# Optimization experiments

Hardware: AMD Instinct MI355X
Metric: run time of the kernel (lower is better)

## Reference

```python
import jax, jax.numpy as jnp
import numpy as np
from jax import lax

DN3D = ('NDHWC', 'DHWIO', 'NDHWC')


def _conv3d(x, w):
    return lax.conv_general_dilated(x, w, window_strides=(1, 1, 1),
                                    padding='VALID', dimension_numbers=DN3D)


def _cconv3d(xr, xi, wr, wi):
    # (xr + i xi) * (wr + i wi)
    yr = _conv3d(xr, wr) - _conv3d(xi, wi)
    yi = _conv3d(xr, wi) + _conv3d(xi, wr)
    return yr, yi


def _project(wr, wi, zero_mean):
    # zero-mean + bound-norm weight projection over (kD,kH,kW,Cin) per output filter
    ax = (0, 1, 2, 3)
    if zero_mean:
        wr = wr - jnp.mean(wr, ax, keepdims=True)
        wi = wi - jnp.mean(wi, ax, keepdims=True)
    norm = jnp.sqrt(jnp.sum(wr * wr + wi * wi, ax, keepdims=True))
    s = 1.0 / jnp.maximum(norm, 1.0)
    return wr * s, wi * s


def _sympad(x, pads):
    # pads: list of (lo, hi) per axis
    return jnp.pad(x, pads, mode='symmetric')


def setup_inputs() -> dict:
    key = jax.random.key(0)
    ks = jax.random.split(key, 6)
    B, T, Z, Y, X, C = 2, 8, 20, 64, 64, 2
    F1, F = 32, 32
    return {
        'xr': jax.random.normal(ks[0], (B, T, Z, Y, X, C), jnp.float32),
        'xi': jax.random.normal(ks[1], (B, T, Z, Y, X, C), jnp.float32),
        'wxyz_r': jax.random.normal(ks[2], (3, 3, 3, C, F1), jnp.float32) * 0.1,
        'wxyz_i': jax.random.normal(ks[3], (3, 3, 3, C, F1), jnp.float32) * 0.1,
        'wt_r': jax.random.normal(ks[4], (3, 1, 1, F1, F), jnp.float32) * 0.1,
        'wt_i': jax.random.normal(ks[5], (3, 1, 1, F1, F), jnp.float32) * 0.1,
    }


def reference(xr, xi, wxyz_r, wxyz_i, wt_r, wt_i):
    B, T, Z, Y, X, C = xr.shape
    kz, ky, kx = wxyz_r.shape[0], wxyz_r.shape[1], wxyz_r.shape[2]
    kt = wt_r.shape[0]
    F1 = wxyz_r.shape[-1]
    F = wt_r.shape[-1]

    # projected (zero-mean, bound-norm) complex kernels
    wsr, wsi = _project(wxyz_r, wxyz_i, zero_mean=True)
    wtr, wti = _project(wt_r, wt_i, zero_mean=False)

    # --- spatial 3D conv over (Z,Y,X): fold T into batch (== per-T-slice loop)
    sr = xr.reshape(B * T, Z, Y, X, C)
    si = xi.reshape(B * T, Z, Y, X, C)
    pads_sp = [(0, 0), (kz // 2, kz // 2), (ky // 2, ky // 2), (kx // 2, kx // 2), (0, 0)]
    sr = _sympad(sr, pads_sp)
    si = _sympad(si, pads_sp)
    spr, spi = _cconv3d(sr, si, wsr, wsi)          # [B*T, Z, Y, X, F1]
    spr = spr.reshape(B, T, Z, Y, X, F1)
    spi = spi.reshape(B, T, Z, Y, X, F1)

    # --- temporal conv (kt,1,1) over (T,Z,Y): fold X into batch (== per-X-slice loop)
    tr = spr.transpose(0, 4, 1, 2, 3, 5).reshape(B * X, T, Z, Y, F1)
    ti = spi.transpose(0, 4, 1, 2, 3, 5).reshape(B * X, T, Z, Y, F1)
    pads_t = [(0, 0), (kt // 2, kt // 2), (0, 0), (0, 0), (0, 0)]
    tr = _sympad(tr, pads_t)
    ti = _sympad(ti, pads_t)
    ytr, yti = _cconv3d(tr, ti, wtr, wti)          # [B*X, T, Z, Y, F]
    yr = ytr.reshape(B, X, T, Z, Y, F).transpose(0, 2, 3, 4, 1, 5)
    yi = yti.reshape(B, X, T, Z, Y, F).transpose(0, 2, 3, 4, 1, 5)
    return yr, yi
```

## Files before the change

### kernel.cpp

```cpp
#include <hip/hip_runtime.h>

#define B_ 2
#define T_ 8
#define Z_ 20
#define Y_ 64
#define X_ 64
#define C_ 2
#define F1_ 32
#define F_ 32

constexpr int NPTS = B_*T_*Z_*Y_*X_;
constexpr int ZYX  = Z_*Y_*X_;

constexpr int RING_STRIDE = 36;
constexpr int SLOT_DW     = 16*RING_STRIDE;
constexpr int HALO2       = 3*3*34;

using bf8   = __attribute__((ext_vector_type(8))) short;
using f32x4 = __attribute__((ext_vector_type(4))) float;

__device__ inline unsigned short f2bf(float x) {
    unsigned u = __builtin_bit_cast(unsigned, x);
    return (unsigned short)((u + 0x7fff + ((u >> 16) & 1)) >> 16);
}
__device__ inline unsigned pk(float a, float b) {
    return (unsigned)f2bf(a) | ((unsigned)f2bf(b) << 16);
}

__global__ __launch_bounds__(64) void project_kernel(
    const float* __restrict__ wxr, const float* __restrict__ wxi,
    const float* __restrict__ wtr, const float* __restrict__ wti,
    float* __restrict__ psr, float* __restrict__ psi,
    float* __restrict__ otr, float* __restrict__ oti)
{
    const int bid  = blockIdx.x;
    const int lane = threadIdx.x;

    if (bid < F1_) {
        const int f = bid;
        float er = 0.f, ei = 0.f;
        if (lane < 54) { er = wxr[lane*F1_ + f]; ei = wxi[lane*F1_ + f]; }
        float sr = er, si = ei;
        #pragma unroll
        for (int o = 32; o >= 1; o >>= 1) { sr += __shfl_xor(sr, o); si += __shfl_xor(si, o); }
        const float mr = sr * (1.f/54.f), mi = si * (1.f/54.f);
        const float dr = er - mr, di = ei - mi;
        float sq = (lane < 54) ? (dr*dr + di*di) : 0.f;
        #pragma unroll
        for (int o = 32; o >= 1; o >>= 1) sq += __shfl_xor(sq, o);
        const float s = 1.f / fmaxf(sqrtf(sq), 1.f);
        if (lane < 54) { psr[lane*F1_ + f] = dr*s; psi[lane*F1_ + f] = di*s; }
    } else {
        const int f = bid - F1_;
        float er[2], ei[2];
        float sq = 0.f;
        #pragma unroll
        for (int k = 0; k < 2; ++k) {
            const int e = lane + k*64;
            if (e < 96) { er[k] = wtr[e*F_ + f]; ei[k] = wti[e*F_ + f]; sq += er[k]*er[k] + ei[k]*ei[k]; }
            else        { er[k] = 0.f;  ei[k] = 0.f; }
        }
        #pragma unroll
        for (int o = 32; o >= 1; o >>= 1) sq += __shfl_xor(sq, o);
        const float s = 1.f / fmaxf(sqrtf(sq), 1.f);
        #pragma unroll
        for (int k = 0; k < 2; ++k) {
            const int e = lane + k*64;
            if (e < 96) { otr[e*F_ + f] = er[k]*s; oti[e*F_ + f] = ei[k]*s; }
        }
    }
}

__global__ __launch_bounds__(256) void pack_kernel(
    const float* __restrict__ psr, const float* __restrict__ psi,
    const float* __restrict__ ptr_, const float* __restrict__ pti,
    unsigned short* __restrict__ wsp, unsigned short* __restrict__ wp)
{
    const int g = blockIdx.x;
    if (g < 16) {
        for (int o = g*512 + threadIdx.x; o < (g+1)*512; o += 256) {
            const int j  = o & 7;
            const int l  = (o >> 3) & 63;
            const int gg = o >> 9;
            const int kb = gg & 3, ct = gg >> 2;
            const int k  = kb*32 + (l >> 4)*8 + j;
            const int n  = ct*16 + (l & 15);
            float v = 0.f;
            if (k < 108) {
                const int tap = k >> 2, q = k & 3, cin = q & 1, cp = q >> 1;
                const int f  = n & 31;
                const float wr = psr[(tap*2 + cin)*F1_ + f];
                const float wi = psi[(tap*2 + cin)*F1_ + f];
                v = (n < 32) ? (cp ? -wi : wr) : (cp ? wr : wi);
            }
            wsp[o] = f2bf(v);
        }
    } else {
        for (int o = (g-16)*512 + threadIdx.x; o < (g-15)*512; o += 256) {
            const int j  = o & 7;
            const int l  = (o >> 3) & 63;
            const int gg = o >> 9;
            const int kb = gg % 6, ct = gg / 6;
            const int k  = kb*32 + (l >> 4)*8 + j;
            const int n  = ct*16 + (l & 15);
            const int kt = k >> 6, f1 = (k >> 1) & 31, c = k & 1;
            const int f  = n & 31;
            const float wr = ptr_[(kt*F1_ + f1)*F_ + f];
            const float wi = pti[(kt*F1_ + f1)*F_ + f];
            const float v  = (n < 32) ? (c ? -wi : wr) : (c ? wr : wi);
            wp[o] = f2bf(v);
        }
    }
}

__global__ __launch_bounds__(256) void repack_kernel(
    const float* __restrict__ xr, const float* __restrict__ xi,
    uint2* __restrict__ xb)
{
    const int p = blockIdx.x*256 + threadIdx.x;
    const float2 vr = *reinterpret_cast<const float2*>(xr + (size_t)p*2);
    const float2 vi = *reinterpret_cast<const float2*>(xi + (size_t)p*2);
    uint2 v;
    v.x = (unsigned)f2bf(vr.x) | ((unsigned)f2bf(vr.y) << 16);
    v.y = (unsigned)f2bf(vi.x) | ((unsigned)f2bf(vi.y) << 16);
    xb[p] = v;
}

__global__ __launch_bounds__(256, 2) void fused_kernel(
    const uint2* __restrict__ xb,
    const unsigned short* __restrict__ wsp,
    const unsigned short* __restrict__ wp,
    float* __restrict__ yr, float* __restrict__ yi)
{
    __shared__ uint4 ring4[4*2*3*SLOT_DW/4];
    __shared__ uint2 slab[4][2][HALO2];
    unsigned* ring = reinterpret_cast<unsigned*>(ring4);

    const int tid  = threadIdx.x;
    const int lane = tid & 63;
    const int wid  = tid >> 6;
    const int lx   = lane & 15;
    const int lg   = lane >> 4;

    const int bq    = blockIdx.x;
    const int ypair = bq & 31;
    const int z     = (bq >> 5) % Z_;
    const int b     = bq / (32*Z_);
    const int y     = ypair*2 + (wid >> 1);
    const int x0    = (wid & 1) * 32;

    bf8 wsf[4][4];
    const bf8* w8 = reinterpret_cast<const bf8*>(wsp);
    #pragma unroll
    for (int ct = 0; ct < 4; ++ct)
        #pragma unroll
        for (int kb = 0; kb < 4; ++kb)
            wsf[ct][kb] = w8[(ct*4 + kb)*64 + lane];

    bf8 wtf[4][6];
    const bf8* wp8 = reinterpret_cast<const bf8*>(wp);
    #pragma unroll
    for (int ct = 0; ct < 4; ++ct)
        #pragma unroll
        for (int kb = 0; kb < 6; ++kb)
            wtf[ct][kb] = wp8[(ct*6 + kb)*64 + lane];

    int xoff[5];
    #pragma unroll
    for (int i = 0; i < 5; ++i) {
        int it = lane + i*64; if (it >= HALO2) it = HALO2-1;
        const int iz = it / 102;
        const int iy = (it / 34) % 3;
        const int ix = it % 34;
        int zz = z + iz - 1;  zz = zz < 0 ? 0 : (zz >= Z_ ? Z_-1 : zz);
        int yy = y + iy - 1;  yy = yy < 0 ? 0 : (yy >= Y_ ? Y_-1 : yy);
        int xx = x0 + ix - 1; xx = xx < 0 ? 0 : (xx >= X_ ? X_-1 : xx);
        xoff[i] = (zz*Y_ + yy)*X_ + xx;
    }

    int o8[4][2];
    #pragma unroll
    for (int kb = 0; kb < 4; ++kb)
        #pragma unroll
        for (int s = 0; s < 2; ++s) {
            int ta = kb*8 + lg*2 + s; if (ta > 26) ta = 26;
            const int dz = ta/9, dyx = ta - dz*9, dy = dyx/3, dx = dyx - dy*3;
            o8[kb][s] = (dz*3 + dy)*34 + dx + lx;
        }

    unsigned* myring  = ring + wid*(2*3*SLOT_DW);
    const int  rbase  = lx*RING_STRIDE + lg*4;
    const size_t orow = (((size_t)b*T_)*Z_ + z)*(size_t)(Y_*X_) + (size_t)y*X_ + x0 + lx;

    uint4 caLo, caHi, cbLo, cbHi;
    uint2 stmp[5];

    auto STAGE_ISSUE = [&](int t) {
        const uint2* xt = xb + (size_t)(b*T_ + t)*ZYX;
        #pragma unroll
        for (int i = 0; i < 4; ++i) stmp[i] = xt[xoff[i]];
        if (lane < HALO2 - 256) stmp[4] = xt[xoff[4]];
    };
    auto STAGE_WRITE = [&](int bufsel) {
        uint2* s = slab[wid][bufsel];
        #pragma unroll
        for (int i = 0; i < 4; ++i) s[lane + i*64] = stmp[i];
        if (lane < HALO2 - 256) s[lane + 256] = stmp[4];
    };

    auto SPATIAL = [&](int bufsel, int xadd, uint4& lo, uint4& hi) {
        const uint2* s = slab[wid][bufsel];
        bf8 af[4];
        #pragma unroll
        for (int kb = 0; kb < 4; ++kb) {
            const uint2 l2 = s[o8[kb][0] + xadd];
            const uint2 h2 = s[o8[kb][1] + xadd];
            af[kb] = __builtin_bit_cast(bf8, make_uint4(l2.x, l2.y, h2.x, h2.y));
        }
        f32x4 acc[4];
        #pragma unroll
        for (int ct = 0; ct < 4; ++ct) acc[ct] = (f32x4){0.f,0.f,0.f,0.f};
        #pragma unroll
        for (int ct = 0; ct < 4; ++ct)
            #pragma unroll
            for (int kb = 0; kb < 4; ++kb)
                acc[ct] = __builtin_amdgcn_mfma_f32_16x16x32_bf16(
                              wsf[ct][kb], af[kb], acc[ct], 0, 0, 0);
        lo = make_uint4(pk(acc[0][0],acc[2][0]), pk(acc[0][1],acc[2][1]),
                        pk(acc[0][2],acc[2][2]), pk(acc[0][3],acc[2][3]));
        hi = make_uint4(pk(acc[1][0],acc[3][0]), pk(acc[1][1],acc[3][1]),
                        pk(acc[1][2],acc[3][2]), pk(acc[1][3],acc[3][3]));
    };

    auto WRITE = [&](int tsel, int t, const uint4& lo, const uint4& hi) {
        unsigned* s = myring + tsel*(3*SLOT_DW) + (t % 3)*SLOT_DW + rbase;
        *reinterpret_cast<uint4*>(s)      = lo;
        *reinterpret_cast<uint4*>(s + 16) = hi;
    };

    auto EMIT = [&](int tsel, const uint4& clo, const uint4& chi,
                    int sa, int sb, int tout) {
        const unsigned* tb = myring + tsel*(3*SLOT_DW);
        const unsigned* pa = tb + (sa % 3)*SLOT_DW + rbase;
        const unsigned* pb = tb + (sb % 3)*SLOT_DW + rbase;
        bf8 fr[6];
        fr[0] = __builtin_bit_cast(bf8, *reinterpret_cast<const uint4*>(pa));
        fr[1] = __builtin_bit_cast(bf8, *reinterpret_cast<const uint4*>(pa + 16));
        fr[2] = __builtin_bit_cast(bf8, *reinterpret_cast<const uint4*>(pb));
        fr[3] = __builtin_bit_cast(bf8, *reinterpret_cast<const uint4*>(pb + 16));
        fr[4] = __builtin_bit_cast(bf8, clo);
        fr[5] = __builtin_bit_cast(bf8, chi);
        f32x4 acc[4];
        #pragma unroll
        for (int ct = 0; ct < 4; ++ct) acc[ct] = (f32x4){0.f,0.f,0.f,0.f};
        #pragma unroll
        for (int ct = 0; ct < 4; ++ct)
            #pragma unroll
            for (int kb = 0; kb < 6; ++kb)
                acc[ct] = __builtin_amdgcn_mfma_f32_16x16x32_bf16(
                              wtf[ct][kb], fr[kb], acc[ct], 0, 0, 0);
        const size_t p = orow + tsel*16 + (size_t)tout * ZYX;
        #pragma unroll
        for (int ct = 0; ct < 4; ++ct) {
            float* outp = (ct < 2) ? yr : yi;
            *reinterpret_cast<f32x4*>(outp + p*F_ + (ct & 1)*16 + lg*4) = acc[ct];
        }
    };

    STAGE_ISSUE(0);
    STAGE_WRITE(0);
    STAGE_ISSUE(1);
    SPATIAL(0, 0,  caLo, caHi);
    SPATIAL(0, 16, cbLo, cbHi);
    WRITE(0, 0, caLo, caHi);
    WRITE(1, 0, cbLo, cbHi);

    #pragma unroll 1
    for (int t = 1; t < T_; ++t) {
        STAGE_WRITE(t & 1);
        if (t < T_-1) STAGE_ISSUE(t+1);
        const int sa = t-2 < 0 ? 0 : t-2;
        SPATIAL(t & 1, 0,  caLo, caHi);
        SPATIAL(t & 1, 16, cbLo, cbHi);
        EMIT(0, caLo, caHi, sa, t-1, t-1);
        EMIT(1, cbLo, cbHi, sa, t-1, t-1);
        WRITE(0, t, caLo, caHi);
        WRITE(1, t, cbLo, cbHi);
    }
    EMIT(0, caLo, caHi, T_-2, T_-1, T_-1);
    EMIT(1, cbLo, cbHi, T_-2, T_-1, T_-1);
}

extern "C" void kernel_launch(void* const* d_in, const int* in_sizes, int n_in,
                              void* d_out, int out_size, void* d_ws, size_t ws_size,
                              hipStream_t stream)
{
    const float* xr  = (const float*)d_in[0];
    const float* xi  = (const float*)d_in[1];
    const float* wxr = (const float*)d_in[2];
    const float* wxi = (const float*)d_in[3];
    const float* wtr = (const float*)d_in[4];
    const float* wti = (const float*)d_in[5];

    float* ws   = (float*)d_ws;
    float* psr  = ws;
    float* psi  = ws + 2048;
    float* ptr_ = ws + 4096;
    float* pti  = ws + 8192;
    unsigned short* wsp = (unsigned short*)(ws + 12288);
    unsigned short* wp  = (unsigned short*)(ws + 16384);
    uint2* xb           = (uint2*)(ws + 32768);

    float* yr = (float*)d_out;
    float* yi = yr + (size_t)NPTS * F_;

    hipLaunchKernelGGL(project_kernel, dim3(64), dim3(64), 0, stream,
                       wxr, wxi, wtr, wti, psr, psi, ptr_, pti);
    hipLaunchKernelGGL(pack_kernel, dim3(40), dim3(256), 0, stream,
                       psr, psi, ptr_, pti, wsp, wp);
    hipLaunchKernelGGL(repack_kernel, dim3(NPTS/256), dim3(256), 0, stream,
                       xr, xi, xb);
    hipLaunchKernelGGL(fused_kernel, dim3(B_*Z_*(Y_/2)), dim3(256), 0, stream,
                       xb, wsp, wp, yr, yi);
}
```

Measured before the change: 91.91 us.

## Fuse input bf16 conversion into main kernel and merge weight prep kernels

Removes the separate repack pass that converted the fp32 inputs to a packed bf16 buffer. The fused kernel now loads fp32 real and imaginary values directly and converts them while writing its shared-memory slab. Weight projection and packing are merged into one single-block kernel that keeps intermediates in shared memory, and fused-kernel block indices are remapped to interleave work. This saves a full write and read of the input plus two launches, but doubles the bytes each halo load fetches and serializes weight prep onto one block.

```diff
diff --git a/kernel.cpp b/kernel.cpp
--- a/kernel.cpp
+++ b/kernel.cpp
@@ -27,17 +27,20 @@
     return (unsigned)f2bf(a) | ((unsigned)f2bf(b) << 16);
 }
 
-__global__ __launch_bounds__(64) void project_kernel(
+__global__ __launch_bounds__(256) void prep_kernel(
     const float* __restrict__ wxr, const float* __restrict__ wxi,
     const float* __restrict__ wtr, const float* __restrict__ wti,
-    float* __restrict__ psr, float* __restrict__ psi,
-    float* __restrict__ otr, float* __restrict__ oti)
+    unsigned short* __restrict__ wsp, unsigned short* __restrict__ wp)
 {
-    const int bid  = blockIdx.x;
-    const int lane = threadIdx.x;
-
-    if (bid < F1_) {
-        const int f = bid;
+    __shared__ float s_psr[54*F1_], s_psi[54*F1_];
+    __shared__ float s_ptr[96*F_],  s_pti[96*F_];
+
+    const int tid  = threadIdx.x;
+    const int lane = tid & 63;
+    const int w    = tid >> 6;
+
+    for (int i = 0; i < 8; ++i) {
+        const int f = w*8 + i;
         float er = 0.f, ei = 0.f;
         if (lane < 54) { er = wxr[lane*F1_ + f]; ei = wxi[lane*F1_ + f]; }
         float sr = er, si = ei;
@@ -49,9 +52,11 @@
         #pragma unroll
         for (int o = 32; o >= 1; o >>= 1) sq += __shfl_xor(sq, o);
         const float s = 1.f / fmaxf(sqrtf(sq), 1.f);
-        if (lane < 54) { psr[lane*F1_ + f] = dr*s; psi[lane*F1_ + f] = di*s; }
-    } else {
-        const int f = bid - F1_;
+        if (lane < 54) { s_psr[lane*F1_ + f] = dr*s; s_psi[lane*F1_ + f] = di*s; }
+    }
+
+    for (int i = 0; i < 8; ++i) {
+        const int f = w*8 + i;
         float er[2], ei[2];
         float sq = 0.f;
         #pragma unroll
@@ -66,68 +71,47 @@
         #pragma unroll
         for (int k = 0; k < 2; ++k) {
             const int e = lane + k*64;
-            if (e < 96) { otr[e*F_ + f] = er[k]*s; oti[e*F_ + f] = ei[k]*s; }
-        }
-    }
-}
-
-__global__ __launch_bounds__(256) void pack_kernel(
-    const float* __restrict__ psr, const float* __restrict__ psi,
-    const float* __restrict__ ptr_, const float* __restrict__ pti,
-    unsigned short* __restrict__ wsp, unsigned short* __restrict__ wp)
-{
-    const int g = blockIdx.x;
-    if (g < 16) {
-        for (int o = g*512 + threadIdx.x; o < (g+1)*512; o += 256) {
-            const int j  = o & 7;
-            const int l  = (o >> 3) & 63;
-            const int gg = o >> 9;
-            const int kb = gg & 3, ct = gg >> 2;
-            const int k  = kb*32 + (l >> 4)*8 + j;
-            const int n  = ct*16 + (l & 15);
-            float v = 0.f;
-            if (k < 108) {
-                const int tap = k >> 2, q = k & 3, cin = q & 1, cp = q >> 1;
-                const int f  = n & 31;
-                const float wr = psr[(tap*2 + cin)*F1_ + f];
-                const float wi = psi[(tap*2 + cin)*F1_ + f];
-                v = (n < 32) ? (cp ? -wi : wr) : (cp ? wr : wi);
-            }
-            wsp[o] = f2bf(v);
-        }
-    } else {
-        for (int o = (g-16)*512 + threadIdx.x; o < (g-15)*512; o += 256) {
-            const int j  = o & 7;
-            const int l  = (o >> 3) & 63;
-            const int gg = o >> 9;
-            const int kb = gg % 6, ct = gg / 6;
-            const int k  = kb*32 + (l >> 4)*8 + j;
-            const int n  = ct*16 + (l & 15);
-            const int kt = k >> 6, f1 = (k >> 1) & 31, c = k & 1;
+            if (e < 96) { s_ptr[e*F_ + f] = er[k]*s; s_pti[e*F_ + f] = ei[k]*s; }
+        }
+    }
+
+    __syncthreads();
+
+    for (int o = tid; o < 16*64*8; o += 256) {
+        const int j  = o & 7;
+        const int l  = (o >> 3) & 63;
+        const int gg = o >> 9;
+        const int kb = gg & 3, ct = gg >> 2;
+        const int k  = kb*32 + (l >> 4)*8 + j;
+        const int n  = ct*16 + (l & 15);
+        float v = 0.f;
+        if (k < 108) {
+            const int tap = k >> 2, q = k & 3, cin = q & 1, cp = q >> 1;
             const int f  = n & 31;
-            const float wr = ptr_[(kt*F1_ + f1)*F_ + f];
-            const float wi = pti[(kt*F1_ + f1)*F_ + f];
-            const float v  = (n < 32) ? (c ? -wi : wr) : (c ? wr : wi);
-            wp[o] = f2bf(v);
-        }
-    }
-}
-
-__global__ __launch_bounds__(256) void repack_kernel(
+            const float wr_ = s_psr[(tap*2 + cin)*F1_ + f];
+            const float wi_ = s_psi[(tap*2 + cin)*F1_ + f];
+            v = (n < 32) ? (cp ? -wi_ : wr_) : (cp ? wr_ : wi_);
+        }
+        wsp[o] = f2bf(v);
+    }
+    for (int o = tid; o < 4*6*64*8; o += 256) {
+        const int j  = o & 7;
+        const int l  = (o >> 3) & 63;
+        const int gg = o >> 9;
+        const int kb = gg % 6, ct = gg / 6;
+        const int k  = kb*32 + (l >> 4)*8 + j;
+        const int n  = ct*16 + (l & 15);
+        const int kt = k >> 6, f1 = (k >> 1) & 31, c = k & 1;
+        const int f  = n & 31;
+        const float wr_ = s_ptr[(kt*F1_ + f1)*F_ + f];
+        const float wi_ = s_pti[(kt*F1_ + f1)*F_ + f];
+        const float v   = (n < 32) ? (c ? -wi_ : wr_) : (c ? wr_ : wi_);
+        wp[o] = f2bf(v);
+    }
+}
+
+__global__ __launch_bounds__(256, 2) void fused_kernel(
     const float* __restrict__ xr, const float* __restrict__ xi,
-    uint2* __restrict__ xb)
-{
-    const int p = blockIdx.x*256 + threadIdx.x;
-    const float2 vr = *reinterpret_cast<const float2*>(xr + (size_t)p*2);
-    const float2 vi = *reinterpret_cast<const float2*>(xi + (size_t)p*2);
-    uint2 v;
-    v.x = (unsigned)f2bf(vr.x) | ((unsigned)f2bf(vr.y) << 16);
-    v.y = (unsigned)f2bf(vi.x) | ((unsigned)f2bf(vi.y) << 16);
-    xb[p] = v;
-}
-
-__global__ __launch_bounds__(256, 2) void fused_kernel(
-    const uint2* __restrict__ xb,
     const unsigned short* __restrict__ wsp,
     const unsigned short* __restrict__ wp,
     float* __restrict__ yr, float* __restrict__ yi)
@@ -142,7 +126,7 @@
     const int lx   = lane & 15;
     const int lg   = lane >> 4;
 
-    const int bq    = blockIdx.x;
+    const int bq    = (blockIdx.x & 7)*(1280/8) + (blockIdx.x >> 3);
     const int ypair = bq & 31;
     const int z     = (bq >> 5) % Z_;
     const int b     = bq / (32*Z_);
@@ -193,19 +177,22 @@
     const size_t orow = (((size_t)b*T_)*Z_ + z)*(size_t)(Y_*X_) + (size_t)y*X_ + x0 + lx;
 
     uint4 caLo, caHi, cbLo, cbHi;
-    uint2 stmp[5];
+    float2 str_[5], sti_[5];
 
     auto STAGE_ISSUE = [&](int t) {
-        const uint2* xt = xb + (size_t)(b*T_ + t)*ZYX;
-        #pragma unroll
-        for (int i = 0; i < 4; ++i) stmp[i] = xt[xoff[i]];
-        if (lane < HALO2 - 256) stmp[4] = xt[xoff[4]];
+        const float2* xrt = reinterpret_cast<const float2*>(xr) + (size_t)(b*T_ + t)*ZYX;
+        const float2* xit = reinterpret_cast<const float2*>(xi) + (size_t)(b*T_ + t)*ZYX;
+        #pragma unroll
+        for (int i = 0; i < 4; ++i) { str_[i] = xrt[xoff[i]]; sti_[i] = xit[xoff[i]]; }
+        if (lane < HALO2 - 256) { str_[4] = xrt[xoff[4]]; sti_[4] = xit[xoff[4]]; }
     };
     auto STAGE_WRITE = [&](int bufsel) {
         uint2* s = slab[wid][bufsel];
         #pragma unroll
-        for (int i = 0; i < 4; ++i) s[lane + i*64] = stmp[i];
-        if (lane < HALO2 - 256) s[lane + 256] = stmp[4];
+        for (int i = 0; i < 4; ++i)
+            s[lane + i*64] = make_uint2(pk(str_[i].x, str_[i].y), pk(sti_[i].x, sti_[i].y));
+        if (lane < HALO2 - 256)
+            s[lane + 256] = make_uint2(pk(str_[4].x, str_[4].y), pk(sti_[4].x, sti_[4].y));
     };
 
     auto SPATIAL = [&](int bufsel, int xadd, uint4& lo, uint4& hi) {
@@ -303,23 +290,14 @@
     const float* wti = (const float*)d_in[5];
 
     float* ws   = (float*)d_ws;
-    float* psr  = ws;
-    float* psi  = ws + 2048;
-    float* ptr_ = ws + 4096;
-    float* pti  = ws + 8192;
     unsigned short* wsp = (unsigned short*)(ws + 12288);
     unsigned short* wp  = (unsigned short*)(ws + 16384);
-    uint2* xb           = (uint2*)(ws + 32768);
 
     float* yr = (float*)d_out;
     float* yi = yr + (size_t)NPTS * F_;
 
-    hipLaunchKernelGGL(project_kernel, dim3(64), dim3(64), 0, stream,
-                       wxr, wxi, wtr, wti, psr, psi, ptr_, pti);
-    hipLaunchKernelGGL(pack_kernel, dim3(40), dim3(256), 0, stream,
-                       psr, psi, ptr_, pti, wsp, wp);
-    hipLaunchKernelGGL(repack_kernel, dim3(NPTS/256), dim3(256), 0, stream,
-                       xr, xi, xb);
+    hipLaunchKernelGGL(prep_kernel, dim3(1), dim3(256), 0, stream,
+                       wxr, wxi, wtr, wti, wsp, wp);
     hipLaunchKernelGGL(fused_kernel, dim3(B_*Z_*(Y_/2)), dim3(256), 0, stream,
-                       xb, wsp, wp, yr, yi);
-}
+                       xr, xi, wsp, wp, yr, yi);
+}
```

Result: slower. 157.6 us (+71.5%).
